# Optimization experiments

Hardware: AMD Instinct MI355X
Metric: run time of the kernel (lower is better)

## Reference

```python
import jax, jax.numpy as jnp
import numpy as np

BN_EPS = 1e-5


def _weight_mlp(off, Wh, bh, Wo, bo):
    # off: [Nout, k, 2] relative neighbor offsets -> [Nout, k, 9] interp coeffs
    h = jax.nn.relu(off @ Wh + bh)
    return h @ Wo + bo


def _interp_conv(x, idx, off, Wk, bk, Wh, bh, Wo, bo):
    # x: [B, Cin, Nin]; idx: [Nout, k] neighbor indices into Nin; Wk: [Cout, Cin, 9]
    a = _weight_mlp(off, Wh, bh, Wo, bo)        # [Nout, k, 9]
    feats = x[:, :, idx]                         # gather -> [B, Cin, Nout, k]
    # dynamic filter: per-neighbor kernel = a @ Wk taps, contracted with features
    y = jnp.einsum('nkt,bcnk,oct->bon', a, feats, Wk)  # [B, Cout, Nout]
    return y + bk[None, :, None]


def _bn_relu(x, g, b):
    # BatchNorm1d over [B, C, N] using batch statistics (training-mode forward)
    mean = x.mean(axis=(0, 2), keepdims=True)
    var = x.var(axis=(0, 2), keepdims=True)
    xn = (x - mean) * jax.lax.rsqrt(var + BN_EPS)
    return jax.nn.relu(xn * g[None, :, None] + b[None, :, None])


def setup_inputs() -> dict:
    key = jax.random.key(0)
    ks = jax.random.split(key, 12)
    B, N1, N2, N3, K = 8, 50176, 12544, 3136, 9
    inp = {
        'x': jax.random.normal(ks[0], (B, 3, N1), jnp.float32),
        'nbr1': jax.random.randint(ks[1], (N2, K), 0, N1, jnp.int32),
        'off1': jax.random.normal(ks[2], (N2, K, 2), jnp.float32),
        'nbr2': jax.random.randint(ks[3], (N2, K), 0, N2, jnp.int32),
        'off2': jax.random.normal(ks[4], (N2, K, 2), jnp.float32),
        'pool_idx': jax.random.randint(ks[5], (N3, K), 0, N2, jnp.int32),
        'Wh': jax.random.normal(ks[6], (2, 32), jnp.float32) * 0.5,
        'bh': jnp.zeros((32,), jnp.float32),
        'Wo': jax.random.normal(ks[7], (32, 9), jnp.float32) * 0.2,
        'bo': jnp.zeros((9,), jnp.float32),
        'W1': jax.random.normal(ks[8], (32, 3, 9), jnp.float32) * 0.2,
        'b1': jnp.zeros((32,), jnp.float32),
        'W2': jax.random.normal(ks[9], (32, 32, 9), jnp.float32) * 0.06,
        'b2': jnp.zeros((32,), jnp.float32),
        'W3': jax.random.normal(ks[10], (64, 32, 9), jnp.float32) * 0.06,
        'b3': jnp.zeros((64,), jnp.float32),
        'g1': jnp.ones((32,), jnp.float32), 'be1': jnp.zeros((32,), jnp.float32),
        'g2': jnp.ones((32,), jnp.float32), 'be2': jnp.zeros((32,), jnp.float32),
        'g3': jnp.ones((64,), jnp.float32), 'be3': jnp.zeros((64,), jnp.float32),
    }
    return inp


def reference(x, nbr1, off1, nbr2, off2, pool_idx, Wh, bh, Wo, bo,
              W1, b1, W2, b2, W3, b3, g1, be1, g2, be2, g3, be3):
    x = _bn_relu(_interp_conv(x, nbr1, off1, W1, b1, Wh, bh, Wo, bo), g1, be1)
    x = _bn_relu(_interp_conv(x, nbr2, off2, W2, b2, Wh, bh, Wo, bo), g2, be2)
    x = _bn_relu(_interp_conv(x, nbr2, off2, W3, b3, Wh, bh, Wo, bo), g3, be3)
    # MaxPoolNG: max over irregular neighbor sets from level l2 -> l3
    x = x[:, :, pool_idx].max(axis=-1)           # [B, 64, N3]
    return x
```

## Files before the change

### kernel.cpp

```cpp
#include <hip/hip_runtime.h>
#include <math.h>

#define N1C 50176
#define N2C 12544
#define N3C 3136
#define NT_TILES (N2C * 8 / 64)

typedef __attribute__((ext_vector_type(8))) short bf16x8;
typedef __attribute__((ext_vector_type(4))) float f32x4;

__device__ __forceinline__ unsigned short f2bf(float f) {
    unsigned u = __builtin_bit_cast(unsigned, f);
    u += 0x7fffu + ((u >> 16) & 1u);
    return (unsigned short)(u >> 16);
}
__device__ __forceinline__ unsigned packbf(float a, float b) {
    return (unsigned)f2bf(a) | ((unsigned)f2bf(b) << 16);
}
__device__ __forceinline__ float bf2f(unsigned short u) {
    return __builtin_bit_cast(float, (unsigned)u << 16);
}
__device__ __forceinline__ float bflo(unsigned u) {
    return __builtin_bit_cast(float, u << 16);
}
__device__ __forceinline__ float bfhi(unsigned u) {
    return __builtin_bit_cast(float, u & 0xffff0000u);
}

#define TRB (N1C / 64)
#define MLB (2 * N2C * 9 / 256)
#define PWB 112

__device__ __forceinline__ void pad_one(int i, const float* __restrict__ W,
                                        unsigned short* __restrict__ Wp,
                                        int OC, int CIN, int KT) {
    int j = i & 7;
    int op = (i >> 3) & 31;
    int q = (i >> 8) & 3;
    int kt = (i >> 10) % KT;
    int g = i / (KT * 1024);
    int kp = kt * 32 + q * 8 + j;
    int t = kp / CIN, c = kp - t * CIN;
    int o = g * 32 + op;
    float v = (t < 9 && o < OC) ? W[(o * CIN + c) * 9 + t] : 0.f;
    Wp[i] = f2bf(v);
}

__global__ void prologue_kernel(const float* __restrict__ x, unsigned short* __restrict__ X0,
                                const float* __restrict__ off1, const float* __restrict__ off2,
                                const float* __restrict__ Wh, const float* __restrict__ bh,
                                const float* __restrict__ Wo, const float* __restrict__ bo,
                                float* __restrict__ A1, float* __restrict__ A2,
                                const float* __restrict__ W1, const float* __restrict__ W2,
                                const float* __restrict__ W3,
                                unsigned short* __restrict__ W1p, unsigned short* __restrict__ W2p,
                                unsigned short* __restrict__ W3p) {
    __shared__ float T[64][25];
    int blk = blockIdx.x;
    int tid = threadIdx.x;
    if (blk < TRB) {
        int n0 = blk * 64;
        for (int r = tid; r < 24 * 64; r += 256) {
            int cb = r >> 6;
            int nn = r & 63;
            T[nn][cb] = x[cb * N1C + n0 + nn];
        }
        __syncthreads();
        for (int w = tid; w < 64 * 24; w += 256) {
            int nn = w / 24;
            int u = w - nn * 24;
            X0[(n0 + nn) * 24 + u] = f2bf(T[nn][u]);
        }
    } else if (blk < TRB + MLB) {
        int idx = (blk - TRB) * 256 + tid;
        const float* offp;
        float* Ap;
        if (idx < N2C * 9) { offp = off1 + idx * 2; Ap = A1 + idx * 9; }
        else { int i2 = idx - N2C * 9; offp = off2 + i2 * 2; Ap = A2 + i2 * 9; }
        float o0 = offp[0], o1 = offp[1];
        float out[9];
#pragma unroll
        for (int t = 0; t < 9; t++) out[t] = bo[t];
#pragma unroll
        for (int h = 0; h < 32; h++) {
            float hv = fmaxf(o0 * Wh[h] + o1 * Wh[32 + h] + bh[h], 0.f);
#pragma unroll
            for (int t = 0; t < 9; t++) out[t] += hv * Wo[h * 9 + t];
        }
#pragma unroll
        for (int t = 0; t < 9; t++) Ap[t] = out[t];
    } else {
        int i = (blk - TRB - MLB) * 256 + tid;
        if (i < 1024) pad_one(i, W1, W1p, 32, 3, 1);
        else if (i < 10240) pad_one(i - 1024, W2, W2p, 32, 32, 9);
        else pad_one(i - 10240, W3, W3p, 64, 32, 9);
    }
}

template <int CIN, int MW, bool HAS_BN>
__global__ __launch_bounds__(256, 4)
void conv_kernel(const unsigned short* __restrict__ Xin,
                 const int* __restrict__ nbr,
                 const float* __restrict__ A,
                 const unsigned short* __restrict__ Wp,
                 const float* __restrict__ bias,
                 const float* __restrict__ bnsc,
                 const float* __restrict__ bnsh,
                 unsigned short* __restrict__ Yb,
                 double* __restrict__ Part) {
    constexpr int OC = MW * 16;
    constexpr int KREAL = 9 * CIN;
    constexpr int KROW = (KREAL + 31) & ~31;
    constexpr int KT = KROW / 32;
    constexpr int KSTR = KROW + 8;
    __shared__ alignas(16) short S[64 * KSTR];

    int tid = threadIdx.x;
    int tile = blockIdx.x;
    int n0 = tile * 8;

    if constexpr (KROW != KREAL) {
        for (int i = tid; i < 64 * KSTR; i += 256) S[i] = 0;
        __syncthreads();
    }

    if constexpr (CIN == 3) {
        if (tid < 192) {
            int nsub = tid / 24;
            int u = tid - nsub * 24;
            int b = u / 3, c = u - b * 3;
            int n = n0 + nsub;
            const int* nb = nbr + n * 9;
            const float* Ar = A + n * 81;
            float s[9];
#pragma unroll
            for (int t = 0; t < 9; t++) s[t] = 0.f;
#pragma unroll
            for (int k = 0; k < 9; k++) {
                float f = bf2f(Xin[nb[k] * 24 + u]);
#pragma unroll
                for (int t = 0; t < 9; t++) s[t] = fmaf(Ar[k * 9 + t], f, s[t]);
            }
            int col = nsub * 8 + b;
#pragma unroll
            for (int t = 0; t < 9; t++) S[col * KSTR + t * 3 + c] = (short)f2bf(s[t]);
        }
    } else {
        int nhalf = __builtin_amdgcn_readfirstlane(tid >> 7);
        int rem = tid & 127;
        int b = rem >> 4, c2 = rem & 15;
        float sc0 = 1.f, sh0 = 0.f, sc1 = 1.f, sh1 = 0.f;
        if (HAS_BN) {
            sc0 = bnsc[2 * c2];     sc1 = bnsc[2 * c2 + 1];
            sh0 = bnsh[2 * c2];     sh1 = bnsh[2 * c2 + 1];
        }
        const unsigned* Xu = (const unsigned*)Xin;
        int nbase = n0 + nhalf * 4;
        unsigned fu[36];
#pragma unroll
        for (int g = 0; g < 4; g++)
#pragma unroll
            for (int k = 0; k < 9; k++) {
                int j = nbr[(nbase + g) * 9 + k];
                fu[g * 9 + k] = Xu[(size_t)j * 128 + rem];
            }
#pragma unroll
        for (int g = 0; g < 4; g++) {
            const float* Ar = A + (nbase + g) * 81;
            float s0[9], s1[9];
#pragma unroll
            for (int t = 0; t < 9; t++) { s0[t] = 0.f; s1[t] = 0.f; }
#pragma unroll
            for (int k = 0; k < 9; k++) {
                unsigned u = fu[g * 9 + k];
                float lo = bflo(u), hi = bfhi(u);
                if (HAS_BN) {
                    lo = fmaxf(fmaf(lo, sc0, sh0), 0.f);
                    hi = fmaxf(fmaf(hi, sc1, sh1), 0.f);
                }
#pragma unroll
                for (int t = 0; t < 9; t++) {
                    float a = Ar[k * 9 + t];
                    s0[t] = fmaf(a, lo, s0[t]);
                    s1[t] = fmaf(a, hi, s1[t]);
                }
            }
            int col = (nhalf * 4 + g) * 8 + b;
            unsigned* Srow = (unsigned*)&S[col * KSTR];
#pragma unroll
            for (int t = 0; t < 9; t++) Srow[t * 16 + c2] = packbf(s0[t], s1[t]);
        }
    }
    __syncthreads();

    int lane = tid & 63, wv = tid >> 6, q = lane >> 4, cl = lane & 15;
    int colg = wv * 16 + cl;

    const bf16x8* wf = (const bf16x8*)Wp;
    f32x4 acc[MW];
#pragma unroll
    for (int m = 0; m < MW; m++) acc[m] = (f32x4){0.f, 0.f, 0.f, 0.f};
#pragma unroll
    for (int kt = 0; kt < KT; kt++) {
        bf16x8 bfr = *(const bf16x8*)&S[colg * KSTR + kt * 32 + q * 8];
#pragma unroll
        for (int m = 0; m < MW; m++) {
            const bf16x8* wg = wf + (m >> 1) * (KT * 128);
            bf16x8 am = wg[(kt * 4 + q) * 32 + cl + (m & 1) * 16];
            acc[m] = __builtin_amdgcn_mfma_f32_16x16x32_bf16(am, bfr, acc[m], 0, 0, 0);
        }
    }
    __syncthreads();
    double (*redd)[2 * OC] = (double(*)[2 * OC])S;

    int C = tile * 64 + colg;
    float yv[4 * MW];
#pragma unroll
    for (int m = 0; m < MW; m++)
#pragma unroll
        for (int i = 0; i < 4; i++) {
            int o = m * 16 + q * 4 + i;
            float y = acc[m][i] + bias[o];
            yv[m * 4 + i] = y;
            Yb[(size_t)C * OC + o] = f2bf(y);
        }
#pragma unroll
    for (int r = 0; r < 4 * MW; r++) {
        double ps = (double)yv[r];
        double pq = (double)yv[r] * (double)yv[r];
#pragma unroll
        for (int d = 1; d < 16; d <<= 1) {
            ps += __shfl_xor(ps, d);
            pq += __shfl_xor(pq, d);
        }
        if (cl == 0) {
            int o = (r >> 2) * 16 + q * 4 + (r & 3);
            redd[wv][o] = ps;
            redd[wv][OC + o] = pq;
        }
    }
    __syncthreads();
    if (tid < 2 * OC) {
        double v = redd[0][tid] + redd[1][tid] + redd[2][tid] + redd[3][tid];
        Part[(size_t)tid * NT_TILES + tile] = v;
    }
}

__global__ __launch_bounds__(256, 8)
void bn_reduce(const double* __restrict__ Part,
               const float* __restrict__ g, const float* __restrict__ be,
               float* __restrict__ sc, float* __restrict__ sh, int OC) {
    int o = blockIdx.x;
    int tid = threadIdx.x;
    const double* ps = Part + (size_t)o * NT_TILES;
    const double* pq = Part + (size_t)(OC + o) * NT_TILES;
    double s = 0.0, q = 0.0;
    for (int t = tid; t < NT_TILES; t += 256) {
        s += ps[t];
        q += pq[t];
    }
#pragma unroll
    for (int d = 1; d < 64; d <<= 1) {
        s += __shfl_xor(s, d);
        q += __shfl_xor(q, d);
    }
    __shared__ double red[8];
    int wv = tid >> 6;
    if ((tid & 63) == 0) { red[wv] = s; red[4 + wv] = q; }
    __syncthreads();
    if (tid == 0) {
        double S = red[0] + red[1] + red[2] + red[3];
        double Q = red[4] + red[5] + red[6] + red[7];
        double cnt = (double)N2C * 8.0;
        double mean = S / cnt;
        double var = Q / cnt - mean * mean;
        double rs = 1.0 / sqrt(var + 1e-5);
        double scale = (double)g[o] * rs;
        sc[o] = (float)scale;
        sh[o] = (float)((double)be[o] - mean * scale);
    }
}

__global__ __launch_bounds__(512, 4)
void pool_kernel(const unsigned short* __restrict__ Y3, const int* __restrict__ pidx,
                 const float* __restrict__ sc, const float* __restrict__ sh,
                 float* __restrict__ out) {
    int m0 = blockIdx.x * 8;
    int tid = threadIdx.x;
    int o = tid & 63;
    float s = sc[o], h = sh[o];
    float mx[8];
    int jn[9];
#pragma unroll
    for (int k = 0; k < 9; k++) jn[k] = pidx[m0 * 9 + k];
#pragma unroll 1
    for (int mi = 0; mi < 8; mi++) {
        int jc[9];
#pragma unroll
        for (int k = 0; k < 9; k++) jc[k] = jn[k];
        if (mi < 7) {
#pragma unroll
            for (int k = 0; k < 9; k++) jn[k] = pidx[(m0 + mi + 1) * 9 + k];
        }
        float v0 = 0.f;
#pragma unroll
        for (int k = 0; k < 9; k++) {
            float v = bf2f(Y3[(size_t)jc[k] * 512 + tid]);
            v0 = fmaxf(v0, fmaf(v, s, h));
        }
        mx[mi] = fmaxf(v0, 0.f);
    }
    float* op = out + (size_t)tid * 3136 + m0;
#pragma unroll
    for (int mi = 0; mi < 8; mi++) op[mi] = mx[mi];
}

extern "C" void kernel_launch(void* const* d_in, const int* in_sizes, int n_in,
                              void* d_out, int out_size, void* d_ws, size_t ws_size,
                              hipStream_t stream) {
    const float* x    = (const float*)d_in[0];
    const int*   nbr1 = (const int*)d_in[1];
    const float* off1 = (const float*)d_in[2];
    const int*   nbr2 = (const int*)d_in[3];
    const float* off2 = (const float*)d_in[4];
    const int*   pidx = (const int*)d_in[5];
    const float* Wh   = (const float*)d_in[6];
    const float* bh   = (const float*)d_in[7];
    const float* Wo   = (const float*)d_in[8];
    const float* bo   = (const float*)d_in[9];
    const float* W1   = (const float*)d_in[10];
    const float* b1   = (const float*)d_in[11];
    const float* W2   = (const float*)d_in[12];
    const float* b2   = (const float*)d_in[13];
    const float* W3   = (const float*)d_in[14];
    const float* b3   = (const float*)d_in[15];
    const float* g1   = (const float*)d_in[16];
    const float* be1  = (const float*)d_in[17];
    const float* g2   = (const float*)d_in[18];
    const float* be2  = (const float*)d_in[19];
    const float* g3   = (const float*)d_in[20];
    const float* be3  = (const float*)d_in[21];

    char* ws = (char*)d_ws;
    size_t off = 0;
    auto alloc = [&](size_t bytes) -> void* {
        void* p = ws + off;
        off += (bytes + 255) & ~(size_t)255;
        return p;
    };
    unsigned short* X0b = (unsigned short*)alloc((size_t)N1C * 24 * 2);
    float* A1 = (float*)alloc((size_t)N2C * 81 * 4);
    float* A2 = (float*)alloc((size_t)N2C * 81 * 4);
    unsigned short* Y1b = (unsigned short*)alloc((size_t)N2C * 8 * 32 * 2);
    unsigned short* Y2b = (unsigned short*)alloc((size_t)N2C * 8 * 32 * 2);
    unsigned short* Y3b = (unsigned short*)alloc((size_t)N2C * 8 * 64 * 2);
    unsigned short* W1p = (unsigned short*)alloc(32 * 32 * 2);
    unsigned short* W2p = (unsigned short*)alloc(32 * 288 * 2);
    unsigned short* W3p = (unsigned short*)alloc(64 * 288 * 2);
    double* Part  = (double*)alloc((size_t)NT_TILES * 128 * 8);
    float*  scbuf = (float*)alloc(256 * 4);

    float* sc1 = scbuf;       float* sh1 = scbuf + 32;
    float* sc2 = scbuf + 64;  float* sh2 = scbuf + 96;
    float* sc3 = scbuf + 128; float* sh3 = scbuf + 192;

    prologue_kernel<<<TRB + MLB + PWB, 256, 0, stream>>>(
        x, X0b, off1, off2, Wh, bh, Wo, bo, A1, A2, W1, W2, W3, W1p, W2p, W3p);

    conv_kernel<3, 2, false><<<NT_TILES, 256, 0, stream>>>(
        X0b, nbr1, A1, W1p, b1, nullptr, nullptr, Y1b, Part);
    bn_reduce<<<32, 256, 0, stream>>>(Part, g1, be1, sc1, sh1, 32);

    conv_kernel<32, 2, true><<<NT_TILES, 256, 0, stream>>>(
        Y1b, nbr2, A2, W2p, b2, sc1, sh1, Y2b, Part);
    bn_reduce<<<32, 256, 0, stream>>>(Part, g2, be2, sc2, sh2, 32);

    conv_kernel<32, 4, true><<<NT_TILES, 256, 0, stream>>>(
        Y2b, nbr2, A2, W3p, b3, sc2, sh2, Y3b, Part);
    bn_reduce<<<64, 256, 0, stream>>>(Part, g3, be3, sc3, sh3, 64);

    pool_kernel<<<N3C / 8, 512, 0, stream>>>(Y3b, pidx, sc3, sh3, (float*)d_out);
}
```

Before: 215.7 us.

## Fuse BN statistic reduction into conv kernels via last-block atomic counter

Removes the three separate bn_reduce launches. Each conv block bumps an atomic counter, and the last OC blocks to arrive spin until every tile has finished, then each reduces one channel's partials into scale and shift. The change also packs the bf16 output stores into 8-byte writes, does the per-block partial shuffle reductions in float instead of double, and vectorizes the pool kernel to read two channels per thread with 256 threads. It saves launch gaps but adds spin-waiting in the tail blocks and loses some precision in the block-level partial sums.

```diff
diff --git a/kernel.cpp b/kernel.cpp
--- a/kernel.cpp
+++ b/kernel.cpp
@@ -54,10 +54,12 @@
                                 const float* __restrict__ W1, const float* __restrict__ W2,
                                 const float* __restrict__ W3,
                                 unsigned short* __restrict__ W1p, unsigned short* __restrict__ W2p,
-                                unsigned short* __restrict__ W3p) {
+                                unsigned short* __restrict__ W3p,
+                                unsigned* __restrict__ cnt) {
     __shared__ float T[64][25];
     int blk = blockIdx.x;
     int tid = threadIdx.x;
+    if (blk == 0 && tid < 3) cnt[tid] = 0;
     if (blk < TRB) {
         int n0 = blk * 64;
         for (int r = tid; r < 24 * 64; r += 256) {
@@ -107,13 +109,18 @@
                  const float* __restrict__ bnsc,
                  const float* __restrict__ bnsh,
                  unsigned short* __restrict__ Yb,
-                 double* __restrict__ Part) {
+                 double* __restrict__ Part,
+                 const float* __restrict__ g, const float* __restrict__ be,
+                 float* __restrict__ sc_out, float* __restrict__ sh_out,
+                 unsigned* __restrict__ cnt) {
     constexpr int OC = MW * 16;
     constexpr int KREAL = 9 * CIN;
     constexpr int KROW = (KREAL + 31) & ~31;
     constexpr int KT = KROW / 32;
     constexpr int KSTR = KROW + 8;
     __shared__ alignas(16) short S[64 * KSTR];
+    __shared__ unsigned oldsh;
+    __shared__ double red2[8];
 
     int tid = threadIdx.x;
     int tile = blockIdx.x;
@@ -158,21 +165,21 @@
         int nbase = n0 + nhalf * 4;
         unsigned fu[36];
 #pragma unroll
-        for (int g = 0; g < 4; g++)
+        for (int gg = 0; gg < 4; gg++)
 #pragma unroll
             for (int k = 0; k < 9; k++) {
-                int j = nbr[(nbase + g) * 9 + k];
-                fu[g * 9 + k] = Xu[(size_t)j * 128 + rem];
+                int j = nbr[(nbase + gg) * 9 + k];
+                fu[gg * 9 + k] = Xu[(size_t)j * 128 + rem];
             }
 #pragma unroll
-        for (int g = 0; g < 4; g++) {
-            const float* Ar = A + (nbase + g) * 81;
+        for (int gg = 0; gg < 4; gg++) {
+            const float* Ar = A + (nbase + gg) * 81;
             float s0[9], s1[9];
 #pragma unroll
             for (int t = 0; t < 9; t++) { s0[t] = 0.f; s1[t] = 0.f; }
 #pragma unroll
             for (int k = 0; k < 9; k++) {
-                unsigned u = fu[g * 9 + k];
+                unsigned u = fu[gg * 9 + k];
                 float lo = bflo(u), hi = bfhi(u);
                 if (HAS_BN) {
                     lo = fmaxf(fmaf(lo, sc0, sh0), 0.f);
@@ -185,7 +192,7 @@
                     s1[t] = fmaf(a, hi, s1[t]);
                 }
             }
-            int col = (nhalf * 4 + g) * 8 + b;
+            int col = (nhalf * 4 + gg) * 8 + b;
             unsigned* Srow = (unsigned*)&S[col * KSTR];
 #pragma unroll
             for (int t = 0; t < 9; t++) Srow[t * 16 + c2] = packbf(s0[t], s1[t]);
@@ -211,23 +218,26 @@
         }
     }
     __syncthreads();
-    double (*redd)[2 * OC] = (double(*)[2 * OC])S;
+    float (*redf)[2 * OC] = (float(*)[2 * OC])S;
 
     int C = tile * 64 + colg;
     float yv[4 * MW];
 #pragma unroll
-    for (int m = 0; m < MW; m++)
+    for (int m = 0; m < MW; m++) {
 #pragma unroll
         for (int i = 0; i < 4; i++) {
             int o = m * 16 + q * 4 + i;
-            float y = acc[m][i] + bias[o];
-            yv[m * 4 + i] = y;
-            Yb[(size_t)C * OC + o] = f2bf(y);
-        }
+            yv[m * 4 + i] = acc[m][i] + bias[o];
+        }
+        uint2 pk;
+        pk.x = packbf(yv[m * 4 + 0], yv[m * 4 + 1]);
+        pk.y = packbf(yv[m * 4 + 2], yv[m * 4 + 3]);
+        *(uint2*)&Yb[(size_t)C * OC + m * 16 + q * 4] = pk;
+    }
 #pragma unroll
     for (int r = 0; r < 4 * MW; r++) {
-        double ps = (double)yv[r];
-        double pq = (double)yv[r] * (double)yv[r];
+        float ps = yv[r];
+        float pq = yv[r] * yv[r];
 #pragma unroll
         for (int d = 1; d < 16; d <<= 1) {
             ps += __shfl_xor(ps, d);
@@ -235,61 +245,70 @@
         }
         if (cl == 0) {
             int o = (r >> 2) * 16 + q * 4 + (r & 3);
-            redd[wv][o] = ps;
-            redd[wv][OC + o] = pq;
+            redf[wv][o] = ps;
+            redf[wv][OC + o] = pq;
         }
     }
     __syncthreads();
     if (tid < 2 * OC) {
-        double v = redd[0][tid] + redd[1][tid] + redd[2][tid] + redd[3][tid];
+        double v = (double)redf[0][tid] + (double)redf[1][tid] +
+                   (double)redf[2][tid] + (double)redf[3][tid];
         Part[(size_t)tid * NT_TILES + tile] = v;
     }
-}
-
-__global__ __launch_bounds__(256, 8)
-void bn_reduce(const double* __restrict__ Part,
-               const float* __restrict__ g, const float* __restrict__ be,
-               float* __restrict__ sc, float* __restrict__ sh, int OC) {
-    int o = blockIdx.x;
-    int tid = threadIdx.x;
-    const double* ps = Part + (size_t)o * NT_TILES;
-    const double* pq = Part + (size_t)(OC + o) * NT_TILES;
-    double s = 0.0, q = 0.0;
+
+    __threadfence();
+    __syncthreads();
+    if (tid == 0) oldsh = atomicAdd(cnt, 1u);
+    __syncthreads();
+    unsigned old = oldsh;
+    if (old < (unsigned)(NT_TILES - OC) || old >= (unsigned)NT_TILES) return;
+    int o = (int)(old - (unsigned)(NT_TILES - OC));
+    if (tid == 0) {
+        while (__hip_atomic_load(cnt, __ATOMIC_RELAXED, __HIP_MEMORY_SCOPE_AGENT) <
+               (unsigned)NT_TILES)
+            __builtin_amdgcn_s_sleep(2);
+    }
+    __syncthreads();
+    __threadfence();
+    const double* psrow = Part + (size_t)o * NT_TILES;
+    const double* pqrow = Part + (size_t)(OC + o) * NT_TILES;
+    double rs_ = 0.0, rq_ = 0.0;
     for (int t = tid; t < NT_TILES; t += 256) {
-        s += ps[t];
-        q += pq[t];
+        rs_ += psrow[t];
+        rq_ += pqrow[t];
     }
 #pragma unroll
     for (int d = 1; d < 64; d <<= 1) {
-        s += __shfl_xor(s, d);
-        q += __shfl_xor(q, d);
-    }
-    __shared__ double red[8];
-    int wv = tid >> 6;
-    if ((tid & 63) == 0) { red[wv] = s; red[4 + wv] = q; }
+        rs_ += __shfl_xor(rs_, d);
+        rq_ += __shfl_xor(rq_, d);
+    }
+    if (lane == 0) { red2[wv] = rs_; red2[4 + wv] = rq_; }
     __syncthreads();
     if (tid == 0) {
-        double S = red[0] + red[1] + red[2] + red[3];
-        double Q = red[4] + red[5] + red[6] + red[7];
-        double cnt = (double)N2C * 8.0;
-        double mean = S / cnt;
-        double var = Q / cnt - mean * mean;
+        double Sv = red2[0] + red2[1] + red2[2] + red2[3];
+        double Qv = red2[4] + red2[5] + red2[6] + red2[7];
+        double cntd = (double)N2C * 8.0;
+        double mean = Sv / cntd;
+        double var = Qv / cntd - mean * mean;
         double rs = 1.0 / sqrt(var + 1e-5);
         double scale = (double)g[o] * rs;
-        sc[o] = (float)scale;
-        sh[o] = (float)((double)be[o] - mean * scale);
-    }
-}
-
-__global__ __launch_bounds__(512, 4)
+        sc_out[o] = (float)scale;
+        sh_out[o] = (float)((double)be[o] - mean * scale);
+    }
+}
+
+__global__ __launch_bounds__(256, 8)
 void pool_kernel(const unsigned short* __restrict__ Y3, const int* __restrict__ pidx,
                  const float* __restrict__ sc, const float* __restrict__ sh,
                  float* __restrict__ out) {
     int m0 = blockIdx.x * 8;
     int tid = threadIdx.x;
-    int o = tid & 63;
-    float s = sc[o], h = sh[o];
-    float mx[8];
+    int o2 = tid & 31;
+    int b = tid >> 5;
+    float s0 = sc[2 * o2], h0 = sh[2 * o2];
+    float s1 = sc[2 * o2 + 1], h1 = sh[2 * o2 + 1];
+    const unsigned* Y3u = (const unsigned*)Y3;
+    float mx0[8], mx1[8];
     int jn[9];
 #pragma unroll
     for (int k = 0; k < 9; k++) jn[k] = pidx[m0 * 9 + k];
@@ -302,17 +321,23 @@
 #pragma unroll
             for (int k = 0; k < 9; k++) jn[k] = pidx[(m0 + mi + 1) * 9 + k];
         }
-        float v0 = 0.f;
+        float v0 = 0.f, v1 = 0.f;
 #pragma unroll
         for (int k = 0; k < 9; k++) {
-            float v = bf2f(Y3[(size_t)jc[k] * 512 + tid]);
-            v0 = fmaxf(v0, fmaf(v, s, h));
-        }
-        mx[mi] = fmaxf(v0, 0.f);
-    }
-    float* op = out + (size_t)tid * 3136 + m0;
-#pragma unroll
-    for (int mi = 0; mi < 8; mi++) op[mi] = mx[mi];
+            unsigned u = Y3u[(size_t)jc[k] * 256 + tid];
+            v0 = fmaxf(v0, fmaf(bflo(u), s0, h0));
+            v1 = fmaxf(v1, fmaf(bfhi(u), s1, h1));
+        }
+        mx0[mi] = fmaxf(v0, 0.f);
+        mx1[mi] = fmaxf(v1, 0.f);
+    }
+    float* op0 = out + (size_t)(b * 64 + 2 * o2) * 3136 + m0;
+    float* op1 = op0 + 3136;
+#pragma unroll
+    for (int mi = 0; mi < 8; mi++) {
+        op0[mi] = mx0[mi];
+        op1[mi] = mx1[mi];
+    }
 }
 
 extern "C" void kernel_launch(void* const* d_in, const int* in_sizes, int n_in,
@@ -359,25 +384,23 @@
     unsigned short* W3p = (unsigned short*)alloc(64 * 288 * 2);
     double* Part  = (double*)alloc((size_t)NT_TILES * 128 * 8);
     float*  scbuf = (float*)alloc(256 * 4);
+    unsigned* cnt = (unsigned*)alloc(16);
 
     float* sc1 = scbuf;       float* sh1 = scbuf + 32;
     float* sc2 = scbuf + 64;  float* sh2 = scbuf + 96;
     float* sc3 = scbuf + 128; float* sh3 = scbuf + 192;
 
     prologue_kernel<<<TRB + MLB + PWB, 256, 0, stream>>>(
-        x, X0b, off1, off2, Wh, bh, Wo, bo, A1, A2, W1, W2, W3, W1p, W2p, W3p);
+        x, X0b, off1, off2, Wh, bh, Wo, bo, A1, A2, W1, W2, W3, W1p, W2p, W3p, cnt);
 
     conv_kernel<3, 2, false><<<NT_TILES, 256, 0, stream>>>(
-        X0b, nbr1, A1, W1p, b1, nullptr, nullptr, Y1b, Part);
-    bn_reduce<<<32, 256, 0, stream>>>(Part, g1, be1, sc1, sh1, 32);
+        X0b, nbr1, A1, W1p, b1, nullptr, nullptr, Y1b, Part, g1, be1, sc1, sh1, cnt + 0);
 
     conv_kernel<32, 2, true><<<NT_TILES, 256, 0, stream>>>(
-        Y1b, nbr2, A2, W2p, b2, sc1, sh1, Y2b, Part);
-    bn_reduce<<<32, 256, 0, stream>>>(Part, g2, be2, sc2, sh2, 32);
+        Y1b, nbr2, A2, W2p, b2, sc1, sh1, Y2b, Part, g2, be2, sc2, sh2, cnt + 1);
 
     conv_kernel<32, 4, true><<<NT_TILES, 256, 0, stream>>>(
-        Y2b, nbr2, A2, W3p, b3, sc2, sh2, Y3b, Part);
-    bn_reduce<<<64, 256, 0, stream>>>(Part, g3, be3, sc3, sh3, 64);
-
-    pool_kernel<<<N3C / 8, 512, 0, stream>>>(Y3b, pidx, sc3, sh3, (float*)d_out);
-}
+        Y2b, nbr2, A2, W3p, b3, sc2, sh2, Y3b, Part, g3, be3, sc3, sh3, cnt + 2);
+
+    pool_kernel<<<N3C / 8, 256, 0, stream>>>(Y3b, pidx, sc3, sh3, (float*)d_out);
+}
```

Measured after the change: 732.4 us. 3.4x slower.
